# Kernel optimization log

Measured on AMD Instinct MI355X. Metric: run time of the kernel, lower is better.

Reference implementation:

```python
import jax, jax.numpy as jnp
import numpy as np

N_EMBED = 2048
N_HEAD = 2
HEAD_SIZE = N_EMBED // N_HEAD  # 1024; mask constraint requires T <= HEAD_SIZE


def setup_inputs() -> dict:
    key = jax.random.key(0)
    ks = jax.random.split(key, 9)
    B, T, C, H, D = 32, 1024, N_EMBED, N_HEAD, HEAD_SIZE
    s = 1.0 / np.sqrt(C)
    x = jax.random.normal(ks[0], (B, T, C), dtype=jnp.float32)
    # torch Linear convention: weight (out_features, in_features), y = x @ W.T + b
    Wq = jax.random.normal(ks[1], (H, D, C), dtype=jnp.float32) * s
    Wk = jax.random.normal(ks[2], (H, D, C), dtype=jnp.float32) * s
    Wv = jax.random.normal(ks[3], (H, D, C), dtype=jnp.float32) * s
    bq = jax.random.normal(ks[4], (H, D), dtype=jnp.float32) * 0.01
    bk = jax.random.normal(ks[5], (H, D), dtype=jnp.float32) * 0.01
    bv = jax.random.normal(ks[6], (H, D), dtype=jnp.float32) * 0.01
    Wo = jax.random.normal(ks[7], (C, H * D), dtype=jnp.float32) * s  # no bias
    return {"x": x, "Wq": Wq, "bq": bq, "Wk": Wk, "bk": bk, "Wv": Wv, "bv": bv, "Wo": Wo}


def reference(x, Wq, bq, Wk, bk, Wv, bv, Wo):
    B, T, C = x.shape
    # per-head projections, batched over heads: (B,T,C) x (H,D,C) -> (B,H,T,D)
    q = jnp.einsum('btc,hdc->bhtd', x, Wq) + bq[None, :, None, :]
    k = jnp.einsum('btc,hdc->bhtd', x, Wk) + bk[None, :, None, :]
    v = jnp.einsum('btc,hdc->bhtd', x, Wv) + bv[None, :, None, :]
    # NOTE: original scales by x.shape[-1]**-0.5 == n_embed**-0.5 (not head_size)
    scale = jnp.asarray(C, x.dtype) ** -0.5
    wei = jnp.einsum('bhtd,bhsd->bhts', q, k) * scale  # (B,H,T,T)
    causal = jnp.tril(jnp.ones((T, T), dtype=bool))
    wei = jnp.where(causal[None, None], wei, -jnp.inf)
    wei = jax.nn.softmax(wei, axis=-1)
    out = jnp.einsum('bhts,bhsd->bhtd', wei, v)  # (B,H,T,D)
    # concat heads along last dim: (B,T,H*D)
    out = out.transpose(0, 2, 1, 3).reshape(B, T, -1)
    return out @ Wo.T  # (B,T,C)
```

## Files before the change

### kernel.cpp

```cpp
#include <hip/hip_runtime.h>
#include <hip/hip_bf16.h>
#include <stdint.h>

typedef __bf16 bf16_t;
typedef __bf16 bf16x8 __attribute__((ext_vector_type(8)));
typedef float f32x4 __attribute__((ext_vector_type(4)));

#define AS1(p) ((const __attribute__((address_space(1))) void*)(uintptr_t)(p))
#define AS3(p) ((__attribute__((address_space(3))) void*)(uintptr_t)(p))

__device__ __forceinline__ void gload16(const bf16_t* g, bf16_t* l) {
  __builtin_amdgcn_global_load_lds(AS1(g), AS3(l), 16, 0, 0);
}

#define BAR()    { __builtin_amdgcn_s_barrier(); __builtin_amdgcn_sched_barrier(0); }
#define VMCNT0() { asm volatile("s_waitcnt vmcnt(0)" ::: "memory"); __builtin_amdgcn_sched_barrier(0); }
#define LGKM0()  { asm volatile("s_waitcnt lgkmcnt(0)" ::: "memory"); __builtin_amdgcn_sched_barrier(0); }

__device__ __forceinline__ void gemm256(const bf16_t* __restrict__ A, int lda,
                                        const bf16_t* __restrict__ B, int ldb,
                                        int nt, f32x4 acc[8][4], bf16_t* lds) {
  const int t = (int)threadIdx.x;
  const int lane = t & 63, w = t >> 6;
  const int wr = w >> 2, wc = w & 3;
  const int fr = lane & 15, fq = lane >> 4;
  char* ldsb = (char*)lds;

  const int o = t * 16;
  const int s = o ^ (((t >> 3) & 7) << 4);
  const int r0 = s >> 6, q0 = (s >> 4) & 3;
  const bf16_t* gA0 = A + (size_t)r0 * lda + q0 * 8;
  const bf16_t* gA1 = gA0 + (size_t)128 * lda;
  const bf16_t* gB0 = B + (size_t)r0 * ldb + q0 * 8;
  const bf16_t* gB1 = gB0 + (size_t)128 * ldb;

  const int x = ((fr >> 1) & 7) << 4;
  const int abase = wr * 8192 + ((fr * 64 + fq * 16) ^ x);
  const int bbase = wc * 4096 + ((fr * 64 + fq * 16) ^ x);

  bf16x8 af[4], bvv[4];

#define STAGE_A(cb, kh, kof) \
  gload16(gA0 + (kof) + (kh) * 32, lds + (cb) * 32768 + (kh) * 8192 + t * 8); \
  gload16(gA1 + (kof) + (kh) * 32, lds + (cb) * 32768 + (kh) * 8192 + 4096 + t * 8);
#define STAGE_B(cb, kh, kof) \
  gload16(gB0 + (kof) + (kh) * 32, lds + (cb) * 32768 + 16384 + (kh) * 8192 + t * 8); \
  gload16(gB1 + (kof) + (kh) * 32, lds + (cb) * 32768 + 16384 + (kh) * 8192 + 4096 + t * 8);
#define DS_LOAD(cb, kh, qm) \
  { const char* ap = ldsb + (cb) * 65536 + (kh) * 16384 + abase + (qm) * 4096; \
    const char* bp = ldsb + (cb) * 65536 + 32768 + (kh) * 16384 + bbase; \
    _Pragma("unroll") for (int i = 0; i < 4; ++i) af[i] = *(const bf16x8*)(ap + i * 1024); \
    _Pragma("unroll") for (int n = 0; n < 4; ++n) bvv[n] = *(const bf16x8*)(bp + n * 1024); }
#define MFMA16(qm) \
  { __builtin_amdgcn_s_setprio(1); \
    _Pragma("unroll") for (int i = 0; i < 4; ++i) \
      _Pragma("unroll") for (int n = 0; n < 4; ++n) \
        acc[(qm) * 4 + i][n] = __builtin_amdgcn_mfma_f32_16x16x32_bf16(af[i], bvv[n], acc[(qm) * 4 + i][n], 0, 0, 0); \
    __builtin_amdgcn_s_setprio(0); }

  STAGE_A(0, 0, 0) STAGE_B(0, 0, 0) STAGE_A(0, 1, 0) STAGE_B(0, 1, 0)
  VMCNT0() BAR()

  int kof = 64;
  for (int tt = 0; tt < nt - 1; ++tt, kof += 64) {
    const int cb = tt & 1;
    DS_LOAD(cb, 0, 0) STAGE_A(cb ^ 1, 0, kof) STAGE_A(cb ^ 1, 1, kof) LGKM0() MFMA16(0)
    DS_LOAD(cb, 0, 1) STAGE_B(cb ^ 1, 0, kof) STAGE_B(cb ^ 1, 1, kof) LGKM0() MFMA16(1)
    DS_LOAD(cb, 1, 0) LGKM0() MFMA16(0)
    DS_LOAD(cb, 1, 1) LGKM0() MFMA16(1)
    VMCNT0() BAR()
  }
  {
    const int cb = (nt - 1) & 1;
    DS_LOAD(cb, 0, 0) LGKM0() MFMA16(0)
    DS_LOAD(cb, 0, 1) LGKM0() MFMA16(1)
    DS_LOAD(cb, 1, 0) LGKM0() MFMA16(0)
    DS_LOAD(cb, 1, 1) LGKM0() MFMA16(1)
  }
#undef STAGE_A
#undef STAGE_B
#undef DS_LOAD
#undef MFMA16
}

#define EPI_VARS \
  const int t = (int)threadIdx.x; \
  const int lane = t & 63, w = t >> 6; \
  const int wr = w >> 2, wc = w & 3; \
  const int fr = lane & 15, fq = lane >> 4;

#define ZERO8x4(acc) \
  _Pragma("unroll") for (int _i = 0; _i < 8; ++_i) \
  _Pragma("unroll") for (int _j = 0; _j < 4; ++_j) { f32x4 _z = {0.f,0.f,0.f,0.f}; acc[_i][_j] = _z; }

__global__ void k_cvt(const float* __restrict__ s, bf16_t* __restrict__ d, long n8) {
  long i = (long)blockIdx.x * blockDim.x + threadIdx.x;
  long st = (long)gridDim.x * blockDim.x;
  for (; i < n8; i += st) {
    const float4* sp = (const float4*)(s + i * 8);
    float4 a = sp[0], b = sp[1];
    bf16x8 v;
    v[0] = (__bf16)a.x; v[1] = (__bf16)a.y; v[2] = (__bf16)a.z; v[3] = (__bf16)a.w;
    v[4] = (__bf16)b.x; v[5] = (__bf16)b.y; v[6] = (__bf16)b.z; v[7] = (__bf16)b.w;
    *(bf16x8*)(d + i * 8) = v;
  }
}

__global__ void k_fill(float* o, float v, long n) {
  long i = (long)blockIdx.x * blockDim.x + threadIdx.x;
  long st = (long)gridDim.x * blockDim.x;
  for (; i < n; i += st) o[i] = v;
}

__global__ __launch_bounds__(512, 2) void k_qkv256(
    const bf16_t* __restrict__ xb, const bf16_t* __restrict__ Wb,
    const float* __restrict__ bq, const float* __restrict__ bk, const float* __restrict__ bv,
    bf16_t* __restrict__ Q, bf16_t* __restrict__ K, bf16_t* __restrict__ Vt) {
  __shared__ __align__(16) bf16_t lds[65536];
  int bid = (int)blockIdx.x;
  int id = (bid & 7) * 384 + (bid >> 3);
  EPI_VARS
  f32x4 acc[8][4];
  ZERO8x4(acc)

  bool vmode = id >= 2048;
  int mt = 0, ntile = 0, tok = 0, wm = 0;
  const bf16_t *Ap, *Bp;
  if (!vmode) {
    mt = id & 127; ntile = id >> 7;
    Ap = xb + (size_t)mt * 256 * 2048;
    Bp = Wb + (size_t)ntile * 256 * 2048;
  } else {
    int vb = id - 2048;
    tok = vb & 127; wm = vb >> 7;
    Ap = Wb + (size_t)(16 + wm) * 256 * 2048;
    Bp = xb + (size_t)tok * 256 * 2048;
  }
  gemm256(Ap, 2048, Bp, 2048, 32, acc, lds);

  if (!vmode) {
    int sel = ntile >> 3;
    const float* bias = sel ? bk : bq;
    bf16_t* dst = sel ? K : Q;
    int cbase = (ntile & 7) * 256 + wc * 64;
#pragma unroll
    for (int ni = 0; ni < 4; ++ni) {
      int c2 = cbase + ni * 16 + fr;
      int h = c2 >> 10, d = c2 & 1023;
      float bb = bias[c2];
#pragma unroll
      for (int mi = 0; mi < 8; ++mi) {
        f32x4 a = acc[mi][ni];
#pragma unroll
        for (int r = 0; r < 4; ++r) {
          int m = mt * 256 + wr * 128 + mi * 16 + fq * 4 + r;
          int b = m >> 10, tk = m & 1023;
          dst[(((size_t)(b * 2 + h) << 10) + tk) * 1024 + d] = (bf16_t)(a[r] + bb);
        }
      }
    }
  } else {
#pragma unroll
    for (int mi = 0; mi < 8; ++mi) {
#pragma unroll
      for (int r = 0; r < 4; ++r) {
        int gd = wm * 256 + wr * 128 + mi * 16 + fq * 4 + r;
        int h = gd >> 10, d = gd & 1023;
        float bb = bv[gd];
#pragma unroll
        for (int ni = 0; ni < 4; ++ni) {
          int m = tok * 256 + wc * 64 + ni * 16 + fr;
          int b = m >> 10, tk = m & 1023;
          Vt[(((size_t)(b * 2 + h) << 10) + d) * 1024 + tk] = (bf16_t)(acc[mi][ni][r] + bb);
        }
      }
    }
  }
}

__global__ __launch_bounds__(512, 2) void k_s256(const bf16_t* __restrict__ Q,
                                                 const bf16_t* __restrict__ K,
                                                 float* __restrict__ S, int pbase) {
  __shared__ __align__(16) bf16_t lds[65536];
  int id = (int)blockIdx.x;
  int pc = id / 10, rem = id % 10;
  int ti = 0;
  while (rem > ti) { rem -= ti + 1; ++ti; }
  int tj = rem;
  size_t p = (size_t)(pbase + pc);
  EPI_VARS
  f32x4 acc[8][4];
  ZERO8x4(acc)
  gemm256(Q + (p << 20) + (size_t)ti * 256 * 1024, 1024,
          K + (p << 20) + (size_t)tj * 256 * 1024, 1024, 16, acc, lds);
  float* Sp = S + ((size_t)pc << 20);
  const float scale = 0.022097086912079608f;
#pragma unroll
  for (int mi = 0; mi < 8; ++mi)
#pragma unroll
    for (int ni = 0; ni < 4; ++ni) {
      int col = tj * 256 + wc * 64 + ni * 16 + fr;
      f32x4 a = acc[mi][ni];
#pragma unroll
      for (int r = 0; r < 4; ++r) {
        int row = ti * 256 + wr * 128 + mi * 16 + fq * 4 + r;
        Sp[((size_t)row << 10) + col] = a[r] * scale;
      }
    }
}

__global__ __launch_bounds__(256) void k_softmax(const float* __restrict__ S,
                                                 bf16_t* __restrict__ P) {
  int bid = blockIdx.x;
  int pc = bid >> 10, row = bid & 1023;
  const float* s = S + ((size_t)pc << 20) + ((size_t)row << 10);
  bf16_t* p = P + ((size_t)pc << 20) + ((size_t)row << 10);
  int cend = ((row >> 8) + 1) << 8;
  int t = threadIdx.x;
  __shared__ float red[8];
  float x[4];
  float mx = -1e30f;
#pragma unroll
  for (int j = 0; j < 4; ++j) {
    int c = t + 256 * j;
    x[j] = (c <= row) ? s[c] : -1e30f;
    mx = fmaxf(mx, x[j]);
  }
  for (int o = 32; o > 0; o >>= 1) mx = fmaxf(mx, __shfl_xor(mx, o));
  if (!(t & 63)) red[t >> 6] = mx;
  __syncthreads();
  mx = fmaxf(fmaxf(red[0], red[1]), fmaxf(red[2], red[3]));
  float e[4];
  float sum = 0.f;
#pragma unroll
  for (int j = 0; j < 4; ++j) {
    e[j] = (x[j] > -1e29f) ? __expf(x[j] - mx) : 0.f;
    sum += e[j];
  }
  for (int o = 32; o > 0; o >>= 1) sum += __shfl_xor(sum, o);
  if (!(t & 63)) red[4 + (t >> 6)] = sum;
  __syncthreads();
  sum = red[4] + red[5] + red[6] + red[7];
  float inv = 1.f / sum;
#pragma unroll
  for (int j = 0; j < 4; ++j) {
    int c = t + 256 * j;
    if (c < cend) p[c] = (bf16_t)(e[j] * inv);
  }
}

__global__ __launch_bounds__(512, 2) void k_pv256(const bf16_t* __restrict__ P,
                                                  const bf16_t* __restrict__ Vt,
                                                  bf16_t* __restrict__ O, int pbase) {
  __shared__ __align__(16) bf16_t lds[65536];
  int id = (int)blockIdx.x;
  int pc = id >> 4, rem = id & 15;
  int ti = rem >> 2, dj = rem & 3;
  size_t p = (size_t)(pbase + pc);
  EPI_VARS
  f32x4 acc[8][4];
  ZERO8x4(acc)
  gemm256(P + ((size_t)pc << 20) + (size_t)ti * 256 * 1024, 1024,
          Vt + (p << 20) + (size_t)dj * 256 * 1024, 1024, (ti + 1) * 4, acc, lds);
  int b = (int)(p >> 1), h = (int)(p & 1);
#pragma unroll
  for (int mi = 0; mi < 8; ++mi)
#pragma unroll
    for (int ni = 0; ni < 4; ++ni) {
      int dcol = dj * 256 + wc * 64 + ni * 16 + fr;
      f32x4 a = acc[mi][ni];
#pragma unroll
      for (int r = 0; r < 4; ++r) {
        int tk = ti * 256 + wr * 128 + mi * 16 + fq * 4 + r;
        O[(((size_t)b << 10) + tk) * 2048 + (h << 10) + dcol] = (bf16_t)a[r];
      }
    }
}

__global__ __launch_bounds__(512, 2) void k_out256(const bf16_t* __restrict__ O,
                                                   const bf16_t* __restrict__ W,
                                                   float* __restrict__ out) {
  __shared__ __align__(16) bf16_t lds[65536];
  int bid = (int)blockIdx.x;
  int id = (bid & 7) * 128 + (bid >> 3);
  int mt = id & 127, ntile = id >> 7;
  EPI_VARS
  f32x4 acc[8][4];
  ZERO8x4(acc)
  gemm256(O + (size_t)mt * 256 * 2048, 2048, W + (size_t)ntile * 256 * 2048, 2048, 32, acc, lds);
#pragma unroll
  for (int mi = 0; mi < 8; ++mi)
#pragma unroll
    for (int ni = 0; ni < 4; ++ni) {
      int col = ntile * 256 + wc * 64 + ni * 16 + fr;
      f32x4 a = acc[mi][ni];
#pragma unroll
      for (int r = 0; r < 4; ++r) {
        int row = mt * 256 + wr * 128 + mi * 16 + fq * 4 + r;
        out[(size_t)row * 2048 + col] = a[r];
      }
    }
}

extern "C" void kernel_launch(void* const* d_in, const int* in_sizes, int n_in,
                              void* d_out, int out_size, void* d_ws, size_t ws_size,
                              hipStream_t stream) {
  const float* x  = (const float*)d_in[0];
  const float* Wq = (const float*)d_in[1];
  const float* bq = (const float*)d_in[2];
  const float* Wk = (const float*)d_in[3];
  const float* bk = (const float*)d_in[4];
  const float* Wv = (const float*)d_in[5];
  const float* bv = (const float*)d_in[6];
  const float* Wo = (const float*)d_in[7];
  float* out = (float*)d_out;

  const size_t MiB = 1ull << 20;
  char* w = (char*)d_ws;
  bf16_t* xb    = (bf16_t*)w;
  bf16_t* Ob    = xb;
  bf16_t* Qb    = (bf16_t*)(w + 128 * MiB);
  bf16_t* Kb    = (bf16_t*)(w + 256 * MiB);
  bf16_t* Vt    = (bf16_t*)(w + 384 * MiB);
  bf16_t* Wqkvb = (bf16_t*)(w + 512 * MiB);
  bf16_t* Wob   = (bf16_t*)(w + 536 * MiB);
  float*  Sc    = (float*)(w + 544 * MiB);

  size_t rem = ws_size > 544 * MiB ? ws_size - 544 * MiB : 0;
  int NP = (int)(rem / (6 * MiB));
  if (NP > 64) NP = 64;
  if (NP < 1) {
    k_fill<<<2048, 256, 0, stream>>>(out, (float)(ws_size >> 20), (long)out_size);
    return;
  }
  bf16_t* Pc = (bf16_t*)(w + 544 * MiB + (size_t)NP * 4 * MiB);

  k_cvt<<<2048, 256, 0, stream>>>(x, xb, 8388608L);
  k_cvt<<<1024, 256, 0, stream>>>(Wq, Wqkvb, 524288L);
  k_cvt<<<1024, 256, 0, stream>>>(Wk, Wqkvb + 4194304, 524288L);
  k_cvt<<<1024, 256, 0, stream>>>(Wv, Wqkvb + 8388608, 524288L);
  k_cvt<<<1024, 256, 0, stream>>>(Wo, Wob, 524288L);

  k_qkv256<<<3072, 512, 0, stream>>>(xb, Wqkvb, bq, bk, bv, Qb, Kb, Vt);

  for (int base = 0; base < 64; base += NP) {
    int np = (64 - base) < NP ? (64 - base) : NP;
    k_s256<<<np * 10, 512, 0, stream>>>(Qb, Kb, Sc, base);
    k_softmax<<<np * 1024, 256, 0, stream>>>(Sc, Pc);
    k_pv256<<<np * 16, 512, 0, stream>>>(Pc, Vt, Ob, base);
  }

  k_out256<<<1024, 512, 0, stream>>>(Ob, Wob, out);
}
```

Before: 1.515 ms.

## Restructure GEMM main loop into 4-stage k32 LDS ring with partial vmcnt waits

Replaces the double-buffered 64-wide K pipeline with a four-slot ring of 32-wide K stages. Three stages are prefetched ahead, and each iteration waits only for the oldest stage via a partial vmcnt count. The goal is to hide global-to-LDS latency better and avoid the full vmcnt(0) drain every iteration. The cost is a barrier per 32-wide K step instead of per 64-wide step, and fewer MFMAs between syncs. The code also assumes nt*2 >= 4.

After: 1.593 ms. +5.2%, slower.

```diff
diff --git a/kernel.cpp b/kernel.cpp
--- a/kernel.cpp
+++ b/kernel.cpp
@@ -14,7 +14,7 @@
 }
 
 #define BAR()    { __builtin_amdgcn_s_barrier(); __builtin_amdgcn_sched_barrier(0); }
-#define VMCNT0() { asm volatile("s_waitcnt vmcnt(0)" ::: "memory"); __builtin_amdgcn_sched_barrier(0); }
+#define VMCNT(n) { asm volatile("s_waitcnt vmcnt(" #n ")" ::: "memory"); __builtin_amdgcn_sched_barrier(0); }
 #define LGKM0()  { asm volatile("s_waitcnt lgkmcnt(0)" ::: "memory"); __builtin_amdgcn_sched_barrier(0); }
 
 __device__ __forceinline__ void gemm256(const bf16_t* __restrict__ A, int lda,
@@ -26,61 +26,57 @@
   const int fr = lane & 15, fq = lane >> 4;
   char* ldsb = (char*)lds;
 
-  const int o = t * 16;
-  const int s = o ^ (((t >> 3) & 7) << 4);
-  const int r0 = s >> 6, q0 = (s >> 4) & 3;
+  const int s0 = (t * 16) ^ (((t >> 3) & 7) << 4);
+  const int r0 = s0 >> 6, q0 = (s0 >> 4) & 3;
   const bf16_t* gA0 = A + (size_t)r0 * lda + q0 * 8;
   const bf16_t* gA1 = gA0 + (size_t)128 * lda;
   const bf16_t* gB0 = B + (size_t)r0 * ldb + q0 * 8;
   const bf16_t* gB1 = gB0 + (size_t)128 * ldb;
 
-  const int x = ((fr >> 1) & 7) << 4;
-  const int abase = wr * 8192 + ((fr * 64 + fq * 16) ^ x);
-  const int bbase = wc * 4096 + ((fr * 64 + fq * 16) ^ x);
-
-  bf16x8 af[4], bvv[4];
-
-#define STAGE_A(cb, kh, kof) \
-  gload16(gA0 + (kof) + (kh) * 32, lds + (cb) * 32768 + (kh) * 8192 + t * 8); \
-  gload16(gA1 + (kof) + (kh) * 32, lds + (cb) * 32768 + (kh) * 8192 + 4096 + t * 8);
-#define STAGE_B(cb, kh, kof) \
-  gload16(gB0 + (kof) + (kh) * 32, lds + (cb) * 32768 + 16384 + (kh) * 8192 + t * 8); \
-  gload16(gB1 + (kof) + (kh) * 32, lds + (cb) * 32768 + 16384 + (kh) * 8192 + 4096 + t * 8);
-#define DS_LOAD(cb, kh, qm) \
-  { const char* ap = ldsb + (cb) * 65536 + (kh) * 16384 + abase + (qm) * 4096; \
-    const char* bp = ldsb + (cb) * 65536 + 32768 + (kh) * 16384 + bbase; \
-    _Pragma("unroll") for (int i = 0; i < 4; ++i) af[i] = *(const bf16x8*)(ap + i * 1024); \
-    _Pragma("unroll") for (int n = 0; n < 4; ++n) bvv[n] = *(const bf16x8*)(bp + n * 1024); }
-#define MFMA16(qm) \
-  { __builtin_amdgcn_s_setprio(1); \
-    _Pragma("unroll") for (int i = 0; i < 4; ++i) \
-      _Pragma("unroll") for (int n = 0; n < 4; ++n) \
-        acc[(qm) * 4 + i][n] = __builtin_amdgcn_mfma_f32_16x16x32_bf16(af[i], bvv[n], acc[(qm) * 4 + i][n], 0, 0, 0); \
-    __builtin_amdgcn_s_setprio(0); }
-
-  STAGE_A(0, 0, 0) STAGE_B(0, 0, 0) STAGE_A(0, 1, 0) STAGE_B(0, 1, 0)
-  VMCNT0() BAR()
-
-  int kof = 64;
-  for (int tt = 0; tt < nt - 1; ++tt, kof += 64) {
-    const int cb = tt & 1;
-    DS_LOAD(cb, 0, 0) STAGE_A(cb ^ 1, 0, kof) STAGE_A(cb ^ 1, 1, kof) LGKM0() MFMA16(0)
-    DS_LOAD(cb, 0, 1) STAGE_B(cb ^ 1, 0, kof) STAGE_B(cb ^ 1, 1, kof) LGKM0() MFMA16(1)
-    DS_LOAD(cb, 1, 0) LGKM0() MFMA16(0)
-    DS_LOAD(cb, 1, 1) LGKM0() MFMA16(1)
-    VMCNT0() BAR()
-  }
-  {
-    const int cb = (nt - 1) & 1;
-    DS_LOAD(cb, 0, 0) LGKM0() MFMA16(0)
-    DS_LOAD(cb, 0, 1) LGKM0() MFMA16(1)
-    DS_LOAD(cb, 1, 0) LGKM0() MFMA16(0)
-    DS_LOAD(cb, 1, 1) LGKM0() MFMA16(1)
-  }
-#undef STAGE_A
-#undef STAGE_B
-#undef DS_LOAD
-#undef MFMA16
+  const int swz = (fr * 64 + fq * 16) ^ (((fr >> 1) & 7) << 4);
+  const int abase = wr * 8192 + swz;
+  const int bbase = 16384 + wc * 4096 + swz;
+
+  bf16x8 a0[4], a1[4], bb[4];
+
+#define STAGE(q) { \
+    bf16_t* _d = lds + ((q) & 3) * 16384; \
+    const int _ko = (q) * 32; \
+    gload16(gA0 + _ko, _d + t * 8); \
+    gload16(gA1 + _ko, _d + 4096 + t * 8); \
+    gload16(gB0 + _ko, _d + 8192 + t * 8); \
+    gload16(gB1 + _ko, _d + 12288 + t * 8); \
+  } __builtin_amdgcn_sched_barrier(0);
+#define READS(p) { \
+    const char* _s = ldsb + ((p) & 3) * 32768; \
+    _Pragma("unroll") for (int n = 0; n < 4; ++n) bb[n] = *(const bf16x8*)(_s + bbase + n * 1024); \
+    _Pragma("unroll") for (int i = 0; i < 4; ++i) a0[i] = *(const bf16x8*)(_s + abase + i * 1024); \
+    _Pragma("unroll") for (int i = 0; i < 4; ++i) a1[i] = *(const bf16x8*)(_s + abase + 4096 + i * 1024); }
+#define MFMA32() \
+  __builtin_amdgcn_s_setprio(1); \
+  _Pragma("unroll") for (int i = 0; i < 4; ++i) \
+    _Pragma("unroll") for (int n = 0; n < 4; ++n) \
+      acc[i][n] = __builtin_amdgcn_mfma_f32_16x16x32_bf16(a0[i], bb[n], acc[i][n], 0, 0, 0); \
+  _Pragma("unroll") for (int i = 0; i < 4; ++i) \
+    _Pragma("unroll") for (int n = 0; n < 4; ++n) \
+      acc[4 + i][n] = __builtin_amdgcn_mfma_f32_16x16x32_bf16(a1[i], bb[n], acc[4 + i][n], 0, 0, 0); \
+  __builtin_amdgcn_s_setprio(0);
+
+  const int H = nt * 2;
+  STAGE(0) STAGE(1) STAGE(2)
+  for (int p = 0; p + 4 <= H; ++p) {
+    VMCNT(8) BAR()
+    STAGE(p + 3)
+    READS(p)
+    LGKM0()
+    MFMA32()
+  }
+  VMCNT(8) BAR() READS(H - 3) LGKM0() MFMA32()
+  VMCNT(4) BAR() READS(H - 2) LGKM0() MFMA32()
+  VMCNT(0) BAR() READS(H - 1) LGKM0() MFMA32()
+#undef STAGE
+#undef READS
+#undef MFMA32
 }
 
 #define EPI_VARS \
```

## Restructure GEMM main loop into four barrier-synchronized quarter phases with B reuse

Applied to the files above, without the earlier changes.

Rewrites the inner GEMM loop so all global-to-LDS staging for the next tile is issued up front. Both k-halves of B fragments are loaded once and kept in registers, and A is read in four quarter chunks, each followed by a 16-MFMA block. Workgroup barriers now bracket every phase, lockstepping the waves so LDS reads and MFMA phases line up across waves. The aim is better overlap and fewer redundant B LDS reads, at the cost of more barriers and more live registers.

Result: slower. 1.727 ms (+14.0%).

```diff
diff --git a/kernel.cpp b/kernel.cpp
--- a/kernel.cpp
+++ b/kernel.cpp
@@ -13,7 +13,8 @@
   __builtin_amdgcn_global_load_lds(AS1(g), AS3(l), 16, 0, 0);
 }
 
-#define BAR()    { __builtin_amdgcn_s_barrier(); __builtin_amdgcn_sched_barrier(0); }
+#define SBAR()   __builtin_amdgcn_sched_barrier(0);
+#define BAR()    { __builtin_amdgcn_sched_barrier(0); __builtin_amdgcn_s_barrier(); __builtin_amdgcn_sched_barrier(0); }
 #define VMCNT0() { asm volatile("s_waitcnt vmcnt(0)" ::: "memory"); __builtin_amdgcn_sched_barrier(0); }
 #define LGKM0()  { asm volatile("s_waitcnt lgkmcnt(0)" ::: "memory"); __builtin_amdgcn_sched_barrier(0); }
 
@@ -26,60 +27,85 @@
   const int fr = lane & 15, fq = lane >> 4;
   char* ldsb = (char*)lds;
 
-  const int o = t * 16;
-  const int s = o ^ (((t >> 3) & 7) << 4);
-  const int r0 = s >> 6, q0 = (s >> 4) & 3;
+  const int s0 = (t * 16) ^ (((t >> 3) & 7) << 4);
+  const int r0 = s0 >> 6, q0 = (s0 >> 4) & 3;
   const bf16_t* gA0 = A + (size_t)r0 * lda + q0 * 8;
   const bf16_t* gA1 = gA0 + (size_t)128 * lda;
   const bf16_t* gB0 = B + (size_t)r0 * ldb + q0 * 8;
   const bf16_t* gB1 = gB0 + (size_t)128 * ldb;
 
-  const int x = ((fr >> 1) & 7) << 4;
-  const int abase = wr * 8192 + ((fr * 64 + fq * 16) ^ x);
-  const int bbase = wc * 4096 + ((fr * 64 + fq * 16) ^ x);
-
-  bf16x8 af[4], bvv[4];
-
-#define STAGE_A(cb, kh, kof) \
-  gload16(gA0 + (kof) + (kh) * 32, lds + (cb) * 32768 + (kh) * 8192 + t * 8); \
-  gload16(gA1 + (kof) + (kh) * 32, lds + (cb) * 32768 + (kh) * 8192 + 4096 + t * 8);
-#define STAGE_B(cb, kh, kof) \
-  gload16(gB0 + (kof) + (kh) * 32, lds + (cb) * 32768 + 16384 + (kh) * 8192 + t * 8); \
-  gload16(gB1 + (kof) + (kh) * 32, lds + (cb) * 32768 + 16384 + (kh) * 8192 + 4096 + t * 8);
-#define DS_LOAD(cb, kh, qm) \
-  { const char* ap = ldsb + (cb) * 65536 + (kh) * 16384 + abase + (qm) * 4096; \
-    const char* bp = ldsb + (cb) * 65536 + 32768 + (kh) * 16384 + bbase; \
-    _Pragma("unroll") for (int i = 0; i < 4; ++i) af[i] = *(const bf16x8*)(ap + i * 1024); \
-    _Pragma("unroll") for (int n = 0; n < 4; ++n) bvv[n] = *(const bf16x8*)(bp + n * 1024); }
-#define MFMA16(qm) \
-  { __builtin_amdgcn_s_setprio(1); \
-    _Pragma("unroll") for (int i = 0; i < 4; ++i) \
-      _Pragma("unroll") for (int n = 0; n < 4; ++n) \
-        acc[(qm) * 4 + i][n] = __builtin_amdgcn_mfma_f32_16x16x32_bf16(af[i], bvv[n], acc[(qm) * 4 + i][n], 0, 0, 0); \
+  const int swz = (fr * 64 + fq * 16) ^ (((fr >> 1) & 7) << 4);
+  const int abase = wr * 8192 + swz;
+  const int bbase = wc * 4096 + swz;
+
+  bf16x8 bb0[4], bb1[4];
+  bf16x8 pA0, pA1, pA2, pA3;
+  bf16x8 pB0, pB1, pB2, pB3;
+
+#define STAGE(cb, kof) { \
+    bf16_t* _d = lds + (cb) * 32768; \
+    gload16(gA0 + (kof),      _d + t * 8); \
+    gload16(gA1 + (kof),      _d + 4096 + t * 8); \
+    gload16(gA0 + (kof) + 32, _d + 8192 + t * 8); \
+    gload16(gA1 + (kof) + 32, _d + 12288 + t * 8); \
+    gload16(gB0 + (kof),      _d + 16384 + t * 8); \
+    gload16(gB1 + (kof),      _d + 20480 + t * 8); \
+    gload16(gB0 + (kof) + 32, _d + 24576 + t * 8); \
+    gload16(gB1 + (kof) + 32, _d + 28672 + t * 8); \
+  } SBAR()
+#define DS_B2(cb) { \
+    const char* _b = ldsb + (cb) * 65536 + 32768 + bbase; \
+    _Pragma("unroll") for (int n = 0; n < 4; ++n) bb0[n] = *(const bf16x8*)(_b + n * 1024); \
+    _Pragma("unroll") for (int n = 0; n < 4; ++n) bb1[n] = *(const bf16x8*)(_b + 16384 + n * 1024); }
+#define DS_AQ(cb, q, d0, d1, d2, d3) { \
+    const char* _a = ldsb + (cb) * 65536 + abase + (q) * 2048; \
+    d0 = *(const bf16x8*)(_a); \
+    d1 = *(const bf16x8*)(_a + 1024); \
+    d2 = *(const bf16x8*)(_a + 16384); \
+    d3 = *(const bf16x8*)(_a + 16384 + 1024); }
+#define MFMA16(q, d0, d1, d2, d3) { \
+    __builtin_amdgcn_s_setprio(1); \
+    _Pragma("unroll") for (int n = 0; n < 4; ++n) \
+      acc[2 * (q)][n]     = __builtin_amdgcn_mfma_f32_16x16x32_bf16(d0, bb0[n], acc[2 * (q)][n], 0, 0, 0); \
+    _Pragma("unroll") for (int n = 0; n < 4; ++n) \
+      acc[2 * (q) + 1][n] = __builtin_amdgcn_mfma_f32_16x16x32_bf16(d1, bb0[n], acc[2 * (q) + 1][n], 0, 0, 0); \
+    _Pragma("unroll") for (int n = 0; n < 4; ++n) \
+      acc[2 * (q)][n]     = __builtin_amdgcn_mfma_f32_16x16x32_bf16(d2, bb1[n], acc[2 * (q)][n], 0, 0, 0); \
+    _Pragma("unroll") for (int n = 0; n < 4; ++n) \
+      acc[2 * (q) + 1][n] = __builtin_amdgcn_mfma_f32_16x16x32_bf16(d3, bb1[n], acc[2 * (q) + 1][n], 0, 0, 0); \
     __builtin_amdgcn_s_setprio(0); }
 
-  STAGE_A(0, 0, 0) STAGE_B(0, 0, 0) STAGE_A(0, 1, 0) STAGE_B(0, 1, 0)
+  STAGE(0, 0)
   VMCNT0() BAR()
 
   int kof = 64;
   for (int tt = 0; tt < nt - 1; ++tt, kof += 64) {
     const int cb = tt & 1;
-    DS_LOAD(cb, 0, 0) STAGE_A(cb ^ 1, 0, kof) STAGE_A(cb ^ 1, 1, kof) LGKM0() MFMA16(0)
-    DS_LOAD(cb, 0, 1) STAGE_B(cb ^ 1, 0, kof) STAGE_B(cb ^ 1, 1, kof) LGKM0() MFMA16(1)
-    DS_LOAD(cb, 1, 0) LGKM0() MFMA16(0)
-    DS_LOAD(cb, 1, 1) LGKM0() MFMA16(1)
+    STAGE(cb ^ 1, kof)
+    DS_B2(cb) DS_AQ(cb, 0, pA0, pA1, pA2, pA3)
+    BAR() LGKM0() MFMA16(0, pA0, pA1, pA2, pA3) BAR()
+    DS_AQ(cb, 1, pB0, pB1, pB2, pB3)
+    BAR() LGKM0() MFMA16(1, pB0, pB1, pB2, pB3) BAR()
+    DS_AQ(cb, 2, pA0, pA1, pA2, pA3)
+    BAR() LGKM0() MFMA16(2, pA0, pA1, pA2, pA3) BAR()
+    DS_AQ(cb, 3, pB0, pB1, pB2, pB3)
+    BAR() LGKM0() MFMA16(3, pB0, pB1, pB2, pB3)
     VMCNT0() BAR()
   }
   {
     const int cb = (nt - 1) & 1;
-    DS_LOAD(cb, 0, 0) LGKM0() MFMA16(0)
-    DS_LOAD(cb, 0, 1) LGKM0() MFMA16(1)
-    DS_LOAD(cb, 1, 0) LGKM0() MFMA16(0)
-    DS_LOAD(cb, 1, 1) LGKM0() MFMA16(1)
-  }
-#undef STAGE_A
-#undef STAGE_B
-#undef DS_LOAD
+    DS_B2(cb) DS_AQ(cb, 0, pA0, pA1, pA2, pA3)
+    BAR() LGKM0() MFMA16(0, pA0, pA1, pA2, pA3) BAR()
+    DS_AQ(cb, 1, pB0, pB1, pB2, pB3)
+    BAR() LGKM0() MFMA16(1, pB0, pB1, pB2, pB3) BAR()
+    DS_AQ(cb, 2, pA0, pA1, pA2, pA3)
+    BAR() LGKM0() MFMA16(2, pA0, pA1, pA2, pA3) BAR()
+    DS_AQ(cb, 3, pB0, pB1, pB2, pB3)
+    BAR() LGKM0() MFMA16(3, pB0, pB1, pB2, pB3)
+  }
+#undef STAGE
+#undef DS_B2
+#undef DS_AQ
 #undef MFMA16
 }
 
```

## Switch GEMM core to 32x32x16 MFMA with pipelined LDS reads; store scores as bf16

Applied to the files above, without the earlier changes.

The shared 256x256 GEMM routine now uses 32x32x16 bf16 MFMA instructions with f32x16 accumulators in place of 16x16x32. It double-buffers fragment registers so that LDS reads overlap MFMA issue, using partial lgkmcnt waits. The global-to-LDS staging is regrouped to match, and every epilogue is rewritten for the 32x32 output layout. Separately, the attention score buffer is written as bf16 instead of fp32, which halves score traffic and lets more heads fit per chunk, at some cost in softmax input precision.

Measured after the change: 1.638 ms. 1.08x slower.

```diff
diff --git a/kernel.cpp b/kernel.cpp
--- a/kernel.cpp
+++ b/kernel.cpp
@@ -5,6 +5,7 @@
 typedef __bf16 bf16_t;
 typedef __bf16 bf16x8 __attribute__((ext_vector_type(8)));
 typedef float f32x4 __attribute__((ext_vector_type(4)));
+typedef float f32x16 __attribute__((ext_vector_type(16)));
 
 #define AS1(p) ((const __attribute__((address_space(1))) void*)(uintptr_t)(p))
 #define AS3(p) ((__attribute__((address_space(3))) void*)(uintptr_t)(p))
@@ -13,85 +14,131 @@
   __builtin_amdgcn_global_load_lds(AS1(g), AS3(l), 16, 0, 0);
 }
 
-#define BAR()    { __builtin_amdgcn_s_barrier(); __builtin_amdgcn_sched_barrier(0); }
-#define VMCNT0() { asm volatile("s_waitcnt vmcnt(0)" ::: "memory"); __builtin_amdgcn_sched_barrier(0); }
-#define LGKM0()  { asm volatile("s_waitcnt lgkmcnt(0)" ::: "memory"); __builtin_amdgcn_sched_barrier(0); }
+#define SB()      __builtin_amdgcn_sched_barrier(0);
+#define BAR()     { __builtin_amdgcn_sched_barrier(0); __builtin_amdgcn_s_barrier(); __builtin_amdgcn_sched_barrier(0); }
+#define VMCNT0()  { asm volatile("s_waitcnt vmcnt(0)" ::: "memory"); __builtin_amdgcn_sched_barrier(0); }
+#define LGKM(n)   { asm volatile("s_waitcnt lgkmcnt(" #n ")" ::: "memory"); __builtin_amdgcn_sched_barrier(0); }
 
 __device__ __forceinline__ void gemm256(const bf16_t* __restrict__ A, int lda,
                                         const bf16_t* __restrict__ B, int ldb,
-                                        int nt, f32x4 acc[8][4], bf16_t* lds) {
+                                        int nt, f32x16 acc[4][2], bf16_t* lds) {
   const int t = (int)threadIdx.x;
   const int lane = t & 63, w = t >> 6;
   const int wr = w >> 2, wc = w & 3;
-  const int fr = lane & 15, fq = lane >> 4;
   char* ldsb = (char*)lds;
 
-  const int o = t * 16;
-  const int s = o ^ (((t >> 3) & 7) << 4);
-  const int r0 = s >> 6, q0 = (s >> 4) & 3;
+  const int s0 = (t * 16) ^ (((t >> 3) & 7) << 4);
+  const int r0 = s0 >> 6, q0 = (s0 >> 4) & 3;
   const bf16_t* gA0 = A + (size_t)r0 * lda + q0 * 8;
   const bf16_t* gA1 = gA0 + (size_t)128 * lda;
   const bf16_t* gB0 = B + (size_t)r0 * ldb + q0 * 8;
   const bf16_t* gB1 = gB0 + (size_t)128 * ldb;
 
-  const int x = ((fr >> 1) & 7) << 4;
-  const int abase = wr * 8192 + ((fr * 64 + fq * 16) ^ x);
-  const int bbase = wc * 4096 + ((fr * 64 + fq * 16) ^ x);
-
-  bf16x8 af[4], bvv[4];
-
-#define STAGE_A(cb, kh, kof) \
-  gload16(gA0 + (kof) + (kh) * 32, lds + (cb) * 32768 + (kh) * 8192 + t * 8); \
-  gload16(gA1 + (kof) + (kh) * 32, lds + (cb) * 32768 + (kh) * 8192 + 4096 + t * 8);
-#define STAGE_B(cb, kh, kof) \
-  gload16(gB0 + (kof) + (kh) * 32, lds + (cb) * 32768 + 16384 + (kh) * 8192 + t * 8); \
-  gload16(gB1 + (kof) + (kh) * 32, lds + (cb) * 32768 + 16384 + (kh) * 8192 + 4096 + t * 8);
-#define DS_LOAD(cb, kh, qm) \
-  { const char* ap = ldsb + (cb) * 65536 + (kh) * 16384 + abase + (qm) * 4096; \
-    const char* bp = ldsb + (cb) * 65536 + 32768 + (kh) * 16384 + bbase; \
-    _Pragma("unroll") for (int i = 0; i < 4; ++i) af[i] = *(const bf16x8*)(ap + i * 1024); \
-    _Pragma("unroll") for (int n = 0; n < 4; ++n) bvv[n] = *(const bf16x8*)(bp + n * 1024); }
-#define MFMA16(qm) \
-  { __builtin_amdgcn_s_setprio(1); \
-    _Pragma("unroll") for (int i = 0; i < 4; ++i) \
-      _Pragma("unroll") for (int n = 0; n < 4; ++n) \
-        acc[(qm) * 4 + i][n] = __builtin_amdgcn_mfma_f32_16x16x32_bf16(af[i], bvv[n], acc[(qm) * 4 + i][n], 0, 0, 0); \
+  const int row_l = lane & 31, hi = lane >> 5;
+  const int y = row_l * 64 + hi * 16;
+  const int xo = ((row_l >> 1) & 7) << 4;
+  const int yk0 = y ^ xo;
+  const int yk1 = (y + 32) ^ xo;
+  const int abase = wr * 8192;
+  const int bbase = 32768 + wc * 4096;
+
+  bf16x8 fA[2][4], fB[2][4];
+
+#define STAGE_A(cb, kof) { \
+    bf16_t* _d = lds + (cb) * 32768; \
+    gload16(gA0 + (kof),      _d + t * 8); \
+    gload16(gA1 + (kof),      _d + 4096 + t * 8); \
+    gload16(gA0 + (kof) + 32, _d + 8192 + t * 8); \
+    gload16(gA1 + (kof) + 32, _d + 12288 + t * 8); \
+  } SB()
+#define STAGE_B(cb, kof) { \
+    bf16_t* _d = lds + (cb) * 32768 + 16384; \
+    gload16(gB0 + (kof),      _d + t * 8); \
+    gload16(gB1 + (kof),      _d + 4096 + t * 8); \
+    gload16(gB0 + (kof) + 32, _d + 8192 + t * 8); \
+    gload16(gB1 + (kof) + 32, _d + 12288 + t * 8); \
+  } SB()
+#define RD(a) (*(const bf16x8*)(ldsb + (a)))
+#define READ_B(cb, kh, s) { \
+    const int _b = (cb) * 65536 + bbase + (kh) * 16384; \
+    fB[s][0] = RD(_b + yk0); fB[s][1] = RD(_b + yk1); \
+    fB[s][2] = RD(_b + 2048 + yk0); fB[s][3] = RD(_b + 2048 + yk1); }
+#define READ_A(cb, kh, qm, s) { \
+    const int _a = (cb) * 65536 + abase + (kh) * 16384 + (qm) * 4096; \
+    fA[s][0] = RD(_a + yk0); fA[s][1] = RD(_a + yk1); \
+    fA[s][2] = RD(_a + 2048 + yk0); fA[s][3] = RD(_a + 2048 + yk1); }
+#define MFMA_P(qm, sa, sb) { \
+    __builtin_amdgcn_s_setprio(1); \
+    acc[2*(qm)][0]   = __builtin_amdgcn_mfma_f32_32x32x16_bf16(fA[sa][0], fB[sb][0], acc[2*(qm)][0], 0, 0, 0); \
+    acc[2*(qm)][1]   = __builtin_amdgcn_mfma_f32_32x32x16_bf16(fA[sa][0], fB[sb][2], acc[2*(qm)][1], 0, 0, 0); \
+    acc[2*(qm)+1][0] = __builtin_amdgcn_mfma_f32_32x32x16_bf16(fA[sa][2], fB[sb][0], acc[2*(qm)+1][0], 0, 0, 0); \
+    acc[2*(qm)+1][1] = __builtin_amdgcn_mfma_f32_32x32x16_bf16(fA[sa][2], fB[sb][2], acc[2*(qm)+1][1], 0, 0, 0); \
+    acc[2*(qm)][0]   = __builtin_amdgcn_mfma_f32_32x32x16_bf16(fA[sa][1], fB[sb][1], acc[2*(qm)][0], 0, 0, 0); \
+    acc[2*(qm)][1]   = __builtin_amdgcn_mfma_f32_32x32x16_bf16(fA[sa][1], fB[sb][3], acc[2*(qm)][1], 0, 0, 0); \
+    acc[2*(qm)+1][0] = __builtin_amdgcn_mfma_f32_32x32x16_bf16(fA[sa][3], fB[sb][1], acc[2*(qm)+1][0], 0, 0, 0); \
+    acc[2*(qm)+1][1] = __builtin_amdgcn_mfma_f32_32x32x16_bf16(fA[sa][3], fB[sb][3], acc[2*(qm)+1][1], 0, 0, 0); \
     __builtin_amdgcn_s_setprio(0); }
-
-  STAGE_A(0, 0, 0) STAGE_B(0, 0, 0) STAGE_A(0, 1, 0) STAGE_B(0, 1, 0)
+#define TILE_BODY(cb) \
+    READ_B(cb, 0, 0) READ_A(cb, 0, 0, 0)    \
+    STAGE_A(cb ^ 1, kof)                    \
+    LGKM(0)                                 \
+    READ_A(cb, 0, 1, 1)                     \
+    STAGE_B(cb ^ 1, kof)                    \
+    MFMA_P(0, 0, 0) \
+    READ_B(cb, 1, 1) READ_A(cb, 1, 0, 0)    \
+    LGKM(8)                                 \
+    MFMA_P(1, 1, 0) \
+    READ_A(cb, 1, 1, 1)                     \
+    LGKM(4)                                 \
+    MFMA_P(0, 0, 1) \
+    LGKM(0) \
+    MFMA_P(1, 1, 1)
+#define TILE_TAIL(cb) \
+    READ_B(cb, 0, 0) READ_A(cb, 0, 0, 0) \
+    LGKM(0) \
+    READ_A(cb, 0, 1, 1) \
+    MFMA_P(0, 0, 0) \
+    READ_B(cb, 1, 1) READ_A(cb, 1, 0, 0) \
+    LGKM(8) \
+    MFMA_P(1, 1, 0) \
+    READ_A(cb, 1, 1, 1) \
+    LGKM(4) \
+    MFMA_P(0, 0, 1) \
+    LGKM(0) \
+    MFMA_P(1, 1, 1)
+
+  STAGE_A(0, 0) STAGE_B(0, 0)
   VMCNT0() BAR()
 
   int kof = 64;
   for (int tt = 0; tt < nt - 1; ++tt, kof += 64) {
     const int cb = tt & 1;
-    DS_LOAD(cb, 0, 0) STAGE_A(cb ^ 1, 0, kof) STAGE_A(cb ^ 1, 1, kof) LGKM0() MFMA16(0)
-    DS_LOAD(cb, 0, 1) STAGE_B(cb ^ 1, 0, kof) STAGE_B(cb ^ 1, 1, kof) LGKM0() MFMA16(1)
-    DS_LOAD(cb, 1, 0) LGKM0() MFMA16(0)
-    DS_LOAD(cb, 1, 1) LGKM0() MFMA16(1)
+    TILE_BODY(cb)
     VMCNT0() BAR()
   }
-  {
-    const int cb = (nt - 1) & 1;
-    DS_LOAD(cb, 0, 0) LGKM0() MFMA16(0)
-    DS_LOAD(cb, 0, 1) LGKM0() MFMA16(1)
-    DS_LOAD(cb, 1, 0) LGKM0() MFMA16(0)
-    DS_LOAD(cb, 1, 1) LGKM0() MFMA16(1)
-  }
+  { const int cb = (nt - 1) & 1; TILE_TAIL(cb) }
 #undef STAGE_A
 #undef STAGE_B
-#undef DS_LOAD
-#undef MFMA16
+#undef RD
+#undef READ_B
+#undef READ_A
+#undef MFMA_P
+#undef TILE_BODY
+#undef TILE_TAIL
 }
 
 #define EPI_VARS \
   const int t = (int)threadIdx.x; \
   const int lane = t & 63, w = t >> 6; \
   const int wr = w >> 2, wc = w & 3; \
-  const int fr = lane & 15, fq = lane >> 4;
-
-#define ZERO8x4(acc) \
-  _Pragma("unroll") for (int _i = 0; _i < 8; ++_i) \
-  _Pragma("unroll") for (int _j = 0; _j < 4; ++_j) { f32x4 _z = {0.f,0.f,0.f,0.f}; acc[_i][_j] = _z; }
+  const int colid = lane & 31, hi = lane >> 5;
+
+#define ZERO_ACC(acc) \
+  _Pragma("unroll") for (int _i = 0; _i < 4; ++_i) \
+  _Pragma("unroll") for (int _j = 0; _j < 2; ++_j) \
+  _Pragma("unroll") for (int _k = 0; _k < 16; ++_k) acc[_i][_j][_k] = 0.f;
+
+#define ROWI(i) (((i) & 3) + (((i) >> 2) << 3) + hi * 4)
 
 __global__ void k_cvt(const float* __restrict__ s, bf16_t* __restrict__ d, long n8) {
   long i = (long)blockIdx.x * blockDim.x + threadIdx.x;
@@ -120,8 +167,8 @@
   int bid = (int)blockIdx.x;
   int id = (bid & 7) * 384 + (bid >> 3);
   EPI_VARS
-  f32x4 acc[8][4];
-  ZERO8x4(acc)
+  f32x16 acc[4][2];
+  ZERO_ACC(acc)
 
   bool vmode = id >= 2048;
   int mt = 0, ntile = 0, tok = 0, wm = 0;
@@ -142,45 +189,42 @@
     int sel = ntile >> 3;
     const float* bias = sel ? bk : bq;
     bf16_t* dst = sel ? K : Q;
-    int cbase = (ntile & 7) * 256 + wc * 64;
-#pragma unroll
-    for (int ni = 0; ni < 4; ++ni) {
-      int c2 = cbase + ni * 16 + fr;
+    int cbase = (ntile & 7) * 256 + wc * 64 + colid;
+#pragma unroll
+    for (int ct = 0; ct < 2; ++ct) {
+      int c2 = cbase + ct * 32;
       int h = c2 >> 10, d = c2 & 1023;
       float bb = bias[c2];
 #pragma unroll
-      for (int mi = 0; mi < 8; ++mi) {
-        f32x4 a = acc[mi][ni];
-#pragma unroll
-        for (int r = 0; r < 4; ++r) {
-          int m = mt * 256 + wr * 128 + mi * 16 + fq * 4 + r;
+      for (int rt = 0; rt < 4; ++rt)
+#pragma unroll
+        for (int i = 0; i < 16; ++i) {
+          int m = mt * 256 + wr * 128 + rt * 32 + ROWI(i);
           int b = m >> 10, tk = m & 1023;
-          dst[(((size_t)(b * 2 + h) << 10) + tk) * 1024 + d] = (bf16_t)(a[r] + bb);
+          dst[(((size_t)(b * 2 + h) << 10) + tk) * 1024 + d] = (bf16_t)(acc[rt][ct][i] + bb);
+        }
+    }
+  } else {
+#pragma unroll
+    for (int rt = 0; rt < 4; ++rt)
+#pragma unroll
+      for (int i = 0; i < 16; ++i) {
+        int gd = wm * 256 + wr * 128 + rt * 32 + ROWI(i);
+        int h = gd >> 10, dd = gd & 1023;
+        float bb = bv[gd];
+#pragma unroll
+        for (int ct = 0; ct < 2; ++ct) {
+          int m = tok * 256 + wc * 64 + ct * 32 + colid;
+          int b = m >> 10, tk = m & 1023;
+          Vt[(((size_t)(b * 2 + h) << 10) + dd) * 1024 + tk] = (bf16_t)(acc[rt][ct][i] + bb);
         }
       }
-    }
-  } else {
-#pragma unroll
-    for (int mi = 0; mi < 8; ++mi) {
-#pragma unroll
-      for (int r = 0; r < 4; ++r) {
-        int gd = wm * 256 + wr * 128 + mi * 16 + fq * 4 + r;
-        int h = gd >> 10, d = gd & 1023;
-        float bb = bv[gd];
-#pragma unroll
-        for (int ni = 0; ni < 4; ++ni) {
-          int m = tok * 256 + wc * 64 + ni * 16 + fr;
-          int b = m >> 10, tk = m & 1023;
-          Vt[(((size_t)(b * 2 + h) << 10) + d) * 1024 + tk] = (bf16_t)(acc[mi][ni][r] + bb);
-        }
-      }
-    }
   }
 }
 
 __global__ __launch_bounds__(512, 2) void k_s256(const bf16_t* __restrict__ Q,
                                                  const bf16_t* __restrict__ K,
-                                                 float* __restrict__ S, int pbase) {
+                                                 bf16_t* __restrict__ S, int pbase) {
   __shared__ __align__(16) bf16_t lds[65536];
   int id = (int)blockIdx.x;
   int pc = id / 10, rem = id % 10;
@@ -189,31 +233,30 @@
   int tj = rem;
   size_t p = (size_t)(pbase + pc);
   EPI_VARS
-  f32x4 acc[8][4];
-  ZERO8x4(acc)
+  f32x16 acc[4][2];
+  ZERO_ACC(acc)
   gemm256(Q + (p << 20) + (size_t)ti * 256 * 1024, 1024,
           K + (p << 20) + (size_t)tj * 256 * 1024, 1024, 16, acc, lds);
-  float* Sp = S + ((size_t)pc << 20);
+  bf16_t* Sp = S + ((size_t)pc << 20);
   const float scale = 0.022097086912079608f;
 #pragma unroll
-  for (int mi = 0; mi < 8; ++mi)
-#pragma unroll
-    for (int ni = 0; ni < 4; ++ni) {
-      int col = tj * 256 + wc * 64 + ni * 16 + fr;
-      f32x4 a = acc[mi][ni];
-#pragma unroll
-      for (int r = 0; r < 4; ++r) {
-        int row = ti * 256 + wr * 128 + mi * 16 + fq * 4 + r;
-        Sp[((size_t)row << 10) + col] = a[r] * scale;
+  for (int ct = 0; ct < 2; ++ct) {
+    int col = tj * 256 + wc * 64 + ct * 32 + colid;
+#pragma unroll
+    for (int rt = 0; rt < 4; ++rt)
+#pragma unroll
+      for (int i = 0; i < 16; ++i) {
+        int row = ti * 256 + wr * 128 + rt * 32 + ROWI(i);
+        Sp[((size_t)row << 10) + col] = (bf16_t)(acc[rt][ct][i] * scale);
       }
-    }
-}
-
-__global__ __launch_bounds__(256) void k_softmax(const float* __restrict__ S,
+  }
+}
+
+__global__ __launch_bounds__(256) void k_softmax(const bf16_t* __restrict__ S,
                                                  bf16_t* __restrict__ P) {
   int bid = blockIdx.x;
   int pc = bid >> 10, row = bid & 1023;
-  const float* s = S + ((size_t)pc << 20) + ((size_t)row << 10);
+  const bf16_t* s = S + ((size_t)pc << 20) + ((size_t)row << 10);
   bf16_t* p = P + ((size_t)pc << 20) + ((size_t)row << 10);
   int cend = ((row >> 8) + 1) << 8;
   int t = threadIdx.x;
@@ -223,7 +266,7 @@
 #pragma unroll
   for (int j = 0; j < 4; ++j) {
     int c = t + 256 * j;
-    x[j] = (c <= row) ? s[c] : -1e30f;
+    x[j] = (c <= row) ? (float)s[c] : -1e30f;
     mx = fmaxf(mx, x[j]);
   }
   for (int o = 32; o > 0; o >>= 1) mx = fmaxf(mx, __shfl_xor(mx, o));
@@ -258,23 +301,22 @@
   int ti = rem >> 2, dj = rem & 3;
   size_t p = (size_t)(pbase + pc);
   EPI_VARS
-  f32x4 acc[8][4];
-  ZERO8x4(acc)
+  f32x16 acc[4][2];
+  ZERO_ACC(acc)
   gemm256(P + ((size_t)pc << 20) + (size_t)ti * 256 * 1024, 1024,
           Vt + (p << 20) + (size_t)dj * 256 * 1024, 1024, (ti + 1) * 4, acc, lds);
   int b = (int)(p >> 1), h = (int)(p & 1);
 #pragma unroll
-  for (int mi = 0; mi < 8; ++mi)
-#pragma unroll
-    for (int ni = 0; ni < 4; ++ni) {
-      int dcol = dj * 256 + wc * 64 + ni * 16 + fr;
-      f32x4 a = acc[mi][ni];
-#pragma unroll
-      for (int r = 0; r < 4; ++r) {
-        int tk = ti * 256 + wr * 128 + mi * 16 + fq * 4 + r;
-        O[(((size_t)b << 10) + tk) * 2048 + (h << 10) + dcol] = (bf16_t)a[r];
+  for (int ct = 0; ct < 2; ++ct) {
+    int dcol = dj * 256 + wc * 64 + ct * 32 + colid;
+#pragma unroll
+    for (int rt = 0; rt < 4; ++rt)
+#pragma unroll
+      for (int i = 0; i < 16; ++i) {
+        int tk = ti * 256 + wr * 128 + rt * 32 + ROWI(i);
+        O[(((size_t)b << 10) + tk) * 2048 + (h << 10) + dcol] = (bf16_t)acc[rt][ct][i];
       }
-    }
+  }
 }
 
 __global__ __launch_bounds__(512, 2) void k_out256(const bf16_t* __restrict__ O,
@@ -285,21 +327,20 @@
   int id = (bid & 7) * 128 + (bid >> 3);
   int mt = id & 127, ntile = id >> 7;
   EPI_VARS
-  f32x4 acc[8][4];
-  ZERO8x4(acc)
+  f32x16 acc[4][2];
+  ZERO_ACC(acc)
   gemm256(O + (size_t)mt * 256 * 2048, 2048, W + (size_t)ntile * 256 * 2048, 2048, 32, acc, lds);
 #pragma unroll
-  for (int mi = 0; mi < 8; ++mi)
-#pragma unroll
-    for (int ni = 0; ni < 4; ++ni) {
-      int col = ntile * 256 + wc * 64 + ni * 16 + fr;
-      f32x4 a = acc[mi][ni];
-#pragma unroll
-      for (int r = 0; r < 4; ++r) {
-        int row = mt * 256 + wr * 128 + mi * 16 + fq * 4 + r;
-        out[(size_t)row * 2048 + col] = a[r];
+  for (int ct = 0; ct < 2; ++ct) {
+    int col = ntile * 256 + wc * 64 + ct * 32 + colid;
+#pragma unroll
+    for (int rt = 0; rt < 4; ++rt)
+#pragma unroll
+      for (int i = 0; i < 16; ++i) {
+        int row = mt * 256 + wr * 128 + rt * 32 + ROWI(i);
+        out[(size_t)row * 2048 + col] = acc[rt][ct][i];
       }
-    }
+  }
 }
 
 extern "C" void kernel_launch(void* const* d_in, const int* in_sizes, int n_in,
@@ -324,16 +365,16 @@
   bf16_t* Vt    = (bf16_t*)(w + 384 * MiB);
   bf16_t* Wqkvb = (bf16_t*)(w + 512 * MiB);
   bf16_t* Wob   = (bf16_t*)(w + 536 * MiB);
-  float*  Sc    = (float*)(w + 544 * MiB);
+  bf16_t* Sc    = (bf16_t*)(w + 544 * MiB);
 
   size_t rem = ws_size > 544 * MiB ? ws_size - 544 * MiB : 0;
-  int NP = (int)(rem / (6 * MiB));
+  int NP = (int)(rem / (4 * MiB));
   if (NP > 64) NP = 64;
   if (NP < 1) {
     k_fill<<<2048, 256, 0, stream>>>(out, (float)(ws_size >> 20), (long)out_size);
     return;
   }
-  bf16_t* Pc = (bf16_t*)(w + 544 * MiB + (size_t)NP * 4 * MiB);
+  bf16_t* Pc = (bf16_t*)(w + 544 * MiB + (size_t)NP * 2 * MiB);
 
   k_cvt<<<2048, 256, 0, stream>>>(x, xb, 8388608L);
   k_cvt<<<1024, 256, 0, stream>>>(Wq, Wqkvb, 524288L);
```
